# Kernel tuning notes

Measured on AMD Instinct MI355X. Metric: run time of the kernel, lower is better.

## Reference

```python
import jax, jax.numpy as jnp
import numpy as np

N_NODES = 50000
N_EDGES = 800000
IN_F = 128
HID = 64
HEADS = 4
N_CLASSES = 256
NEG_SLOPE = 0.2


def _gat_layer(h, W, al, ar, b, src, dst, act):
    """One DGL-style GATConv. h:[N,Din], W:[Din,H*F], al/ar:[H,F], b:[H*F].
    Returns [N,H,F]."""
    N = h.shape[0]
    H, F = al.shape
    z = (h @ W).reshape(N, H, F)                       # projected feats
    el = jnp.einsum('nhf,hf->nh', z, al)               # [N,H] src score part
    er = jnp.einsum('nhf,hf->nh', z, ar)               # [N,H] dst score part
    e = jax.nn.leaky_relu(el[src] + er[dst], negative_slope=NEG_SLOPE)  # [E,H]
    # segment softmax over incoming edges of each destination node
    emax = jax.ops.segment_max(e, dst, num_segments=N)                  # [N,H]
    ex = jnp.exp(e - emax[dst])                                         # [E,H]
    den = jax.ops.segment_sum(ex, dst, num_segments=N)                  # [N,H]
    alpha = ex / jnp.maximum(den[dst], 1e-9)                            # [E,H]
    msg = z[src] * alpha[:, :, None]                                    # [E,H,F]
    out = jax.ops.segment_sum(msg, dst, num_segments=N)                 # [N,H,F]
    out = out + b.reshape(1, H, F)
    return act(out) if act is not None else out


def setup_inputs() -> dict:
    key = jax.random.key(0)
    ks = jax.random.split(key, 16)
    feat = jax.random.normal(ks[0], (N_NODES, IN_F), dtype=jnp.float32)
    src = jax.random.randint(ks[1], (N_EDGES,), 0, N_NODES, dtype=jnp.int32)
    dst = jax.random.randint(ks[2], (N_EDGES,), 0, N_NODES, dtype=jnp.int32)

    def glorot(k, shape):
        fan = shape[0] + shape[-1]
        return jax.random.normal(k, shape, dtype=jnp.float32) * np.sqrt(2.0 / fan)

    # layer 0: IN_F -> HEADS*HID
    W0 = glorot(ks[3], (IN_F, HEADS * HID))
    al0 = glorot(ks[4], (HEADS, HID))
    ar0 = glorot(ks[5], (HEADS, HID))
    b0 = jnp.zeros((HEADS * HID,), dtype=jnp.float32)
    # layer 1: HEADS*HID -> HEADS*HID
    W1 = glorot(ks[6], (HEADS * HID, HEADS * HID))
    al1 = glorot(ks[7], (HEADS, HID))
    ar1 = glorot(ks[8], (HEADS, HID))
    b1 = jnp.zeros((HEADS * HID,), dtype=jnp.float32)
    # final layer: HEADS*HID -> HEADS*N_CLASSES
    W2 = glorot(ks[9], (HEADS * HID, HEADS * N_CLASSES))
    al2 = glorot(ks[10], (HEADS, N_CLASSES))
    ar2 = glorot(ks[11], (HEADS, N_CLASSES))
    b2 = jnp.zeros((HEADS * N_CLASSES,), dtype=jnp.float32)
    return {"feat": feat,
            "W0": W0, "al0": al0, "ar0": ar0, "b0": b0,
            "W1": W1, "al1": al1, "ar1": ar1, "b1": b1,
            "W2": W2, "al2": al2, "ar2": ar2, "b2": b2,
            "src": src, "dst": dst}


def reference(feat, W0, al0, ar0, b0, W1, al1, ar1, b1, W2, al2, ar2, b2, src, dst):
    elu = jax.nn.elu
    h = _gat_layer(feat, W0, al0, ar0, b0, src, dst, elu).reshape(N_NODES, -1)
    h = _gat_layer(h, W1, al1, ar1, b1, src, dst, elu).reshape(N_NODES, -1)
    logits = _gat_layer(h, W2, al2, ar2, b2, src, dst, None).mean(axis=1)  # [N, C]
    return logits
```

## Files before the change

kernel.cpp:

```cpp
#include <hip/hip_runtime.h>
#include <hip/hip_bf16.h>


#define NN 50000
#define NE 800000
#define NH_HEADS 4

typedef __attribute__((ext_vector_type(8))) short short8;
typedef __attribute__((ext_vector_type(8))) _Float16 half8;
typedef __attribute__((ext_vector_type(4))) _Float16 half4;
typedef __attribute__((ext_vector_type(4))) float floatx4;

__device__ inline float bf2f(short s) {
    union { unsigned u; float f; } v; v.u = ((unsigned)(unsigned short)s) << 16;
    return v.f;
}
__device__ inline short f2bf_rne(float x) {
    union { float f; unsigned u; } v; v.f = x;
    unsigned r = v.u + 0x7fff + ((v.u >> 16) & 1);
    return (short)(r >> 16);
}
__device__ inline void split1(float x, short& h, short& l) {
    union { float f; unsigned u; } v; v.f = x;
    h = (short)(v.u >> 16);
    union { float f; unsigned u; } rv; rv.f = v.f - bf2f(h);
    l = (short)(rv.u >> 16);
}

__device__ inline void load_lds16(const void* g, void* l) {
    __builtin_amdgcn_global_load_lds(
        (const __attribute__((address_space(1))) void*)g,
        (__attribute__((address_space(3))) void*)l, 16, 0, 0);
}


__global__ void hist_kernel(const int* __restrict__ dst, int* __restrict__ deg, int E) {
    int e = blockIdx.x * 256 + threadIdx.x;
    if (e < E) atomicAdd(&deg[dst[e]], 1);
}

__global__ void scan_block_kernel(const int* __restrict__ deg, int* __restrict__ offs,
                                  int* __restrict__ bsums, int n) {
    __shared__ int s[256];
    int tid = threadIdx.x;
    int i = blockIdx.x * 256 + tid;
    int v = (i < n) ? deg[i] : 0;
    s[tid] = v;
    __syncthreads();
    for (int off = 1; off < 256; off <<= 1) {
        int x = (tid >= off) ? s[tid - off] : 0;
        __syncthreads();
        s[tid] += x;
        __syncthreads();
    }
    if (i < n) offs[i] = s[tid] - v;
    if (tid == 255) bsums[blockIdx.x] = s[255];
}

__global__ void scan_sums_kernel(const int* __restrict__ bsums, int* __restrict__ boffs, int nb) {
    __shared__ int s[256];
    int tid = threadIdx.x;
    int v = (tid < nb) ? bsums[tid] : 0;
    s[tid] = v;
    __syncthreads();
    for (int off = 1; off < 256; off <<= 1) {
        int x = (tid >= off) ? s[tid - off] : 0;
        __syncthreads();
        s[tid] += x;
        __syncthreads();
    }
    boffs[tid] = s[tid] - v;
}

__global__ void add_offs_kernel(int* __restrict__ offs, const int* __restrict__ boffs,
                                int* __restrict__ cursor, int n, int total) {
    int i = blockIdx.x * 256 + threadIdx.x;
    if (i < n) {
        int o = offs[i] + boffs[blockIdx.x];
        offs[i] = o;
        cursor[i] = o;
    }
    if (i == 0) offs[n] = total;
}

__global__ void scatter_kernel(const int* __restrict__ src, const int* __restrict__ dst,
                               int* __restrict__ cursor, int* __restrict__ psrc, int E) {
    int e = blockIdx.x * 256 + threadIdx.x;
    if (e < E) {
        int p = atomicAdd(&cursor[dst[e]], 1);
        psrc[p] = src[e];
    }
}


__global__ __launch_bounds__(256) void splitA_rm(const float* __restrict__ A,
                                                 short* __restrict__ hi,
                                                 short* __restrict__ lo,
                                                 int total8) {
    int tid = blockIdx.x * 256 + threadIdx.x;
    if (tid >= total8) return;
    const float* p = A + (size_t)tid * 8;
    float4 x0 = ((const float4*)p)[0];
    float4 x1 = ((const float4*)p)[1];
    float xs[8] = {x0.x, x0.y, x0.z, x0.w, x1.x, x1.y, x1.z, x1.w};
    short8 hv, lv;
#pragma unroll
    for (int j = 0; j < 8; ++j) { short h, l; split1(xs[j], h, l); hv[j] = h; lv[j] = l; }
    ((short8*)hi)[tid] = hv;
    ((short8*)lo)[tid] = lv;
}


__global__ __launch_bounds__(256) void splitB_kernel(const float* __restrict__ B,
                                                     short* __restrict__ hi,
                                                     short* __restrict__ lo,
                                                     int K, int N) {
    int tid = blockIdx.x * 256 + threadIdx.x;
    int NG = N >> 4;
    int total = (K >> 5) * NG * 64;
    if (tid >= total) return;
    int lane = tid & 63;
    int rc = tid >> 6;
    int g = rc % NG, c = rc / NG;
    int n = g * 16 + (lane & 15);
    int k = c * 32 + (lane >> 4) * 8;
    short8 hv, lv;
#pragma unroll
    for (int j = 0; j < 8; ++j) {
        float x = B[(size_t)(k + j) * N + n];
        short h = f2bf_rne(x);
        hv[j] = h;
        lv[j] = f2bf_rne(x - bf2f(h));
    }
    ((short8*)hi)[tid] = hv;
    ((short8*)lo)[tid] = lv;
}

__global__ __launch_bounds__(256) void splitB_f16_kernel(const float* __restrict__ B,
                                                         _Float16* __restrict__ hi,
                                                         _Float16* __restrict__ lo,
                                                         int K, int N) {
    int tid = blockIdx.x * 256 + threadIdx.x;
    int NG = N >> 4;
    int total = (K >> 5) * NG * 64;
    if (tid >= total) return;
    int lane = tid & 63;
    int rc = tid >> 6;
    int g = rc % NG, c = rc / NG;
    int n = g * 16 + (lane & 15);
    int k = c * 32 + (lane >> 4) * 8;
    half8 hv, lv;
#pragma unroll
    for (int j = 0; j < 8; ++j) {
        float x = B[(size_t)(k + j) * N + n];
        _Float16 h = (_Float16)x;
        hv[j] = h;
        lv[j] = (_Float16)(x - (float)h);
    }
    ((half8*)hi)[tid] = hv;
    ((half8*)lo)[tid] = lv;
}

__global__ __launch_bounds__(256) void splitB2_f16s_kernel(const float* __restrict__ W2,
                                                           _Float16* __restrict__ hi) {
    int tid = blockIdx.x * 256 + threadIdx.x;
    const int NG = 16;
    int total = (1024 >> 5) * NG * 64;
    if (tid >= total) return;
    int lane = tid & 63;
    int rc = tid >> 6;
    int g = rc % NG, c = rc / NG;
    int n = g * 16 + (lane & 15);
    int kk = c * 32 + (lane >> 4) * 8;
    half8 hv;
#pragma unroll
    for (int j = 0; j < 8; ++j) {
        int kg = kk + j;
        int h = kg >> 8, k = kg & 255;
        hv[j] = (_Float16)W2[(size_t)k * 1024 + h * 256 + n];
    }
    ((half8*)hi)[tid] = hv;
}


__device__ inline floatx4 mfma16(short8 a, short8 b, floatx4 c) {
    return __builtin_amdgcn_mfma_f32_16x16x32_bf16(a, b, c, 0, 0, 0);
}
__device__ inline floatx4 mfma16h(half8 a, half8 b, floatx4 c) {
    return __builtin_amdgcn_mfma_f32_16x16x32_f16(a, b, c, 0, 0, 0);
}

__global__ __launch_bounds__(256) void gemm_n256l(const short* __restrict__ Ahi,
                                                  const short* __restrict__ Alo,
                                                  const short* __restrict__ Bh,
                                                  const short* __restrict__ Bl,
                                                  _Float16* __restrict__ Cf,
                                                  const float* __restrict__ alv,
                                                  const float* __restrict__ arv,
                                                  float* __restrict__ elo,
                                                  float* __restrict__ ero,
                                                  int M, int K) {
    int KC = K >> 5;
    __shared__ short AhL[2048];
    __shared__ short AlL[2048];
    int t = threadIdx.x;
    int lane = t & 63;
    int w = t >> 6;
    int bm = blockIdx.x * 64;
    int g0 = w * 4;
    const short8* pBh = (const short8*)Bh;
    const short8* pBl = (const short8*)Bl;

    floatx4 acc[4][4] = {};

    int row = bm + (w << 4) + (lane & 15);
    if (row >= M) row = M - 1;
    const short* gh = Ahi + (size_t)row * K + ((lane >> 4) << 3);
    const short* gl = Alo + (size_t)row * K + ((lane >> 4) << 3);
    short* lh = AhL + w * 512;
    short* ll = AlL + w * 512;

    for (int c = 0; c < KC; ++c) {
        load_lds16(gh + (size_t)c * 32, lh);
        load_lds16(gl + (size_t)c * 32, ll);
        short8 bh[4], bl[4];
#pragma unroll
        for (int g = 0; g < 4; ++g) {
            bh[g] = pBh[((size_t)c * 16 + g0 + g) * 64 + lane];
            bl[g] = pBl[((size_t)c * 16 + g0 + g) * 64 + lane];
        }
        __syncthreads();
#pragma unroll
        for (int mt = 0; mt < 4; ++mt) {
            short8 ah = *(const short8*)(AhL + mt * 512 + lane * 8);
            short8 al = *(const short8*)(AlL + mt * 512 + lane * 8);
#pragma unroll
            for (int g = 0; g < 4; ++g) {
                acc[mt][g] = mfma16(ah, bh[g], acc[mt][g]);
                acc[mt][g] = mfma16(al, bh[g], acc[mt][g]);
                acc[mt][g] = mfma16(ah, bl[g], acc[mt][g]);
            }
        }
        __syncthreads();
    }

    int rowb = bm + (lane >> 4) * 4;
    int colb = w * 64 + (lane & 15);
#pragma unroll
    for (int mt = 0; mt < 4; ++mt) {
#pragma unroll
        for (int r = 0; r < 4; ++r) {
            int rr = rowb + mt * 16 + r;
            if (rr < M) {
#pragma unroll
                for (int g = 0; g < 4; ++g) {
                    Cf[(size_t)rr * 256 + colb + g * 16] = (_Float16)acc[mt][g][r];
                }
            }
        }
    }

    if (alv) {
        float alr[4], arr_[4];
#pragma unroll
        for (int g = 0; g < 4; ++g) {
            int f = w * 64 + (lane & 15) + g * 16;
            alr[g] = alv[f];
            arr_[g] = arv[f];
        }
#pragma unroll
        for (int mt = 0; mt < 4; ++mt) {
#pragma unroll
            for (int r = 0; r < 4; ++r) {
                float se = acc[mt][0][r] * alr[0] + acc[mt][1][r] * alr[1] +
                           acc[mt][2][r] * alr[2] + acc[mt][3][r] * alr[3];
                float sr = acc[mt][0][r] * arr_[0] + acc[mt][1][r] * arr_[1] +
                           acc[mt][2][r] * arr_[2] + acc[mt][3][r] * arr_[3];
                se += __shfl_xor(se, 1); se += __shfl_xor(se, 2);
                se += __shfl_xor(se, 4); se += __shfl_xor(se, 8);
                sr += __shfl_xor(sr, 1); sr += __shfl_xor(sr, 2);
                sr += __shfl_xor(sr, 4); sr += __shfl_xor(sr, 8);
                int rr = rowb + mt * 16 + r;
                if ((lane & 15) == 0 && rr < M) {
                    elo[rr * 4 + w] = se;
                    ero[rr * 4 + w] = sr;
                }
            }
        }
    }
}

__global__ __launch_bounds__(256) void gemm_f16_n256(const _Float16* __restrict__ A,
                                                     const _Float16* __restrict__ Bh,
                                                     const _Float16* __restrict__ Bl,
                                                     const float* __restrict__ bias4,
                                                     float* __restrict__ C,
                                                     _Float16* __restrict__ Cf,
                                                     const float* __restrict__ alv,
                                                     const float* __restrict__ arv,
                                                     float* __restrict__ elo,
                                                     float* __restrict__ ero,
                                                     int M, int K) {
    int KC = K >> 5;
    __shared__ _Float16 AL[2048];
    int t = threadIdx.x;
    int lane = t & 63;
    int w = t >> 6;
    int bm = blockIdx.x * 64;
    int g0 = w * 4;
    const half8* pBh = (const half8*)Bh;
    const half8* pBl = (const half8*)Bl;
    bool dual = (Bl != nullptr);

    floatx4 acc[4][4] = {};

    int row = bm + (w << 4) + (lane & 15);
    if (row >= M) row = M - 1;
    const _Float16* gA = A + (size_t)row * K + ((lane >> 4) << 3);
    _Float16* lA = AL + w * 512;

    for (int c = 0; c < KC; ++c) {
        load_lds16(gA + (size_t)c * 32, lA);
        half8 bh[4], bl[4];
#pragma unroll
        for (int g = 0; g < 4; ++g) {
            bh[g] = pBh[((size_t)c * 16 + g0 + g) * 64 + lane];
        }
        if (dual) {
#pragma unroll
            for (int g = 0; g < 4; ++g) {
                bl[g] = pBl[((size_t)c * 16 + g0 + g) * 64 + lane];
            }
        }
        __syncthreads();
#pragma unroll
        for (int mt = 0; mt < 4; ++mt) {
            half8 a = *(const half8*)(AL + mt * 512 + lane * 8);
#pragma unroll
            for (int g = 0; g < 4; ++g) {
                acc[mt][g] = mfma16h(a, bh[g], acc[mt][g]);
            }
            if (dual) {
#pragma unroll
                for (int g = 0; g < 4; ++g) {
                    acc[mt][g] = mfma16h(a, bl[g], acc[mt][g]);
                }
            }
        }
        __syncthreads();
    }

    int rowb = bm + (lane >> 4) * 4;
    int colb = w * 64 + (lane & 15);
#pragma unroll
    for (int mt = 0; mt < 4; ++mt) {
#pragma unroll
        for (int r = 0; r < 4; ++r) {
            int rr = rowb + mt * 16 + r;
            if (rr < M) {
#pragma unroll
                for (int g = 0; g < 4; ++g) {
                    int col = colb + g * 16;
                    float v = acc[mt][g][r];
                    if (bias4) {
                        v = 0.25f * (v + bias4[col] + bias4[col + 256] +
                                     bias4[col + 512] + bias4[col + 768]);
                    }
                    if (Cf) Cf[(size_t)rr * 256 + col] = (_Float16)v;
                    else    C[(size_t)rr * 256 + col] = v;
                }
            }
        }
    }

    if (alv) {
        float alr[4], arr_[4];
#pragma unroll
        for (int g = 0; g < 4; ++g) {
            int f = w * 64 + (lane & 15) + g * 16;
            alr[g] = alv[f];
            arr_[g] = arv[f];
        }
#pragma unroll
        for (int mt = 0; mt < 4; ++mt) {
#pragma unroll
            for (int r = 0; r < 4; ++r) {
                float se = acc[mt][0][r] * alr[0] + acc[mt][1][r] * alr[1] +
                           acc[mt][2][r] * alr[2] + acc[mt][3][r] * alr[3];
                float sr = acc[mt][0][r] * arr_[0] + acc[mt][1][r] * arr_[1] +
                           acc[mt][2][r] * arr_[2] + acc[mt][3][r] * arr_[3];
                se += __shfl_xor(se, 1); se += __shfl_xor(se, 2);
                se += __shfl_xor(se, 4); se += __shfl_xor(se, 8);
                sr += __shfl_xor(sr, 1); sr += __shfl_xor(sr, 2);
                sr += __shfl_xor(sr, 4); sr += __shfl_xor(sr, 8);
                int rr = rowb + mt * 16 + r;
                if ((lane & 15) == 0 && rr < M) {
                    elo[rr * 4 + w] = se;
                    ero[rr * 4 + w] = sr;
                }
            }
        }
    }
}


__global__ __launch_bounds__(256) void proj_av_kernel(const float* __restrict__ W2,
                                                      const float* __restrict__ al2,
                                                      const float* __restrict__ ar2,
                                                      float* __restrict__ val,
                                                      float* __restrict__ var_) {
    int gid = blockIdx.x * 256 + threadIdx.x;
    int w = gid >> 6;
    int lane = threadIdx.x & 63;
    if (w >= 1024) return;
    int h = w >> 8, k = w & 255;
    const float* wrow = W2 + (size_t)k * 1024 + h * 256;
    const float* ap = al2 + h * 256;
    const float* rp = ar2 + h * 256;
    float sv = 0.f, sr = 0.f;
    for (int j = lane; j < 256; j += 64) {
        float x = wrow[j];
        sv += x * ap[j];
        sr += x * rp[j];
    }
#pragma unroll
    for (int off = 32; off > 0; off >>= 1) {
        sv += __shfl_down(sv, off);
        sr += __shfl_down(sr, off);
    }
    if (lane == 0) { val[w] = sv; var_[w] = sr; }
}

__global__ __launch_bounds__(256) void elr2_kernel(const _Float16* __restrict__ h1,
                                                   const float* __restrict__ val,
                                                   const float* __restrict__ var_,
                                                   float* __restrict__ el,
                                                   float* __restrict__ er) {
    int gid = blockIdx.x * 256 + threadIdx.x;
    int w = gid >> 6;
    int lane = threadIdx.x & 63;
    if (w >= NN * 4) return;
    int n = w >> 2, h = w & 3;
    const _Float16* hr = h1 + (size_t)n * 256;
    const float* vp = val + h * 256;
    const float* rp = var_ + h * 256;
    float se = 0.f, sr = 0.f;
    for (int k = lane; k < 256; k += 64) {
        float x = (float)hr[k];
        se += x * vp[k];
        sr += x * rp[k];
    }
#pragma unroll
    for (int off = 32; off > 0; off >>= 1) {
        se += __shfl_down(se, off);
        sr += __shfl_down(sr, off);
    }
    if (lane == 0) { el[w] = se; er[w] = sr; }
}


__global__ __launch_bounds__(64) void agg_z64_kernel(const _Float16* __restrict__ z,
                                                     const float* __restrict__ el,
                                                     const float* __restrict__ er,
                                                     const int* __restrict__ offs,
                                                     const int* __restrict__ psrc,
                                                     const float* __restrict__ bias,
                                                     _Float16* __restrict__ out) {
    int n = blockIdx.x;
    int l = threadIdx.x;
    __shared__ float p_lds[16][4];
    __shared__ int src_lds[16];
    __shared__ float den_lds[4];
    if (l < 4) den_lds[l] = 0.f;
    int e_local = l >> 2, hh = l & 3;
    int h = l >> 4;
    float er_n = er[n * 4 + hh];
    int beg = offs[n], end = offs[n + 1];
    float a0 = 0.f, a1 = 0.f, a2 = 0.f, a3 = 0.f;
    for (int base = beg; base < end; base += 16) {
        int cnt = min(16, end - base);
        __syncthreads();
        float p = 0.f;
        if (e_local < cnt) {
            int s = psrc[base + e_local];
            if (hh == 0) src_lds[e_local] = s;
            float sc = el[s * 4 + hh] + er_n;
            sc = (sc > 0.f) ? sc : 0.2f * sc;
            p = __expf(sc);
            p_lds[e_local][hh] = p;
        }
        float d = p;
        d += __shfl_xor(d, 4);  d += __shfl_xor(d, 8);
        d += __shfl_xor(d, 16); d += __shfl_xor(d, 32);
        if (l < 4) den_lds[l] += d;
        __syncthreads();
        for (int e = 0; e < cnt; ++e) {
            half4 v = *(const half4*)(z + (size_t)src_lds[e] * 256 + (l << 2));
            float pe = p_lds[e][h];
            a0 += pe * (float)v[0];
            a1 += pe * (float)v[1];
            a2 += pe * (float)v[2];
            a3 += pe * (float)v[3];
        }
    }
    __syncthreads();
    float rd = 1.f / fmaxf(den_lds[h], 1e-9f);
    float vals[4] = {a0, a1, a2, a3};
    half4 o;
#pragma unroll
    for (int j = 0; j < 4; ++j) {
        float x = vals[j] * rd + bias[(l << 2) + j];
        x = (x > 0.f) ? x : (__expf(x) - 1.f);
        o[j] = (_Float16)x;
    }
    *(half4*)(out + (size_t)n * 256 + (l << 2)) = o;
}

__global__ __launch_bounds__(64) void aggH_64_kernel(const _Float16* __restrict__ h1,
                                                     const float* __restrict__ el,
                                                     const float* __restrict__ er,
                                                     const int* __restrict__ offs,
                                                     const int* __restrict__ psrc,
                                                     _Float16* __restrict__ oA) {
    int n = blockIdx.x;
    int l = threadIdx.x;
    __shared__ __align__(16) float p_lds[16][4];
    __shared__ int src_lds[16];
    __shared__ float den_lds[4];
    if (l < 4) den_lds[l] = 0.f;
    int e_local = l >> 2, hh = l & 3;
    float er_n = er[n * 4 + hh];
    int beg = offs[n], end = offs[n + 1];
    float acc[4][4] = {};
    for (int base = beg; base < end; base += 16) {
        int cnt = min(16, end - base);
        __syncthreads();
        float p = 0.f;
        if (e_local < cnt) {
            int s = psrc[base + e_local];
            if (hh == 0) src_lds[e_local] = s;
            float sc = el[s * 4 + hh] + er_n;
            sc = (sc > 0.f) ? sc : 0.2f * sc;
            p = __expf(sc);
            p_lds[e_local][hh] = p;
        }
        float d = p;
        d += __shfl_xor(d, 4);  d += __shfl_xor(d, 8);
        d += __shfl_xor(d, 16); d += __shfl_xor(d, 32);
        if (l < 4) den_lds[l] += d;
        __syncthreads();
        for (int e = 0; e < cnt; ++e) {
            half4 v = *(const half4*)(h1 + (size_t)src_lds[e] * 256 + (l << 2));
            float vf0 = (float)v[0], vf1 = (float)v[1];
            float vf2 = (float)v[2], vf3 = (float)v[3];
            floatx4 pv = *(const floatx4*)&p_lds[e][0];
#pragma unroll
            for (int hd = 0; hd < 4; ++hd) {
                acc[hd][0] += pv[hd] * vf0;
                acc[hd][1] += pv[hd] * vf1;
                acc[hd][2] += pv[hd] * vf2;
                acc[hd][3] += pv[hd] * vf3;
            }
        }
    }
    __syncthreads();
    size_t base_o = (size_t)n * 1024 + (l << 2);
#pragma unroll
    for (int hd = 0; hd < 4; ++hd) {
        float rd = 1.f / fmaxf(den_lds[hd], 1e-9f);
        half4 o;
#pragma unroll
        for (int j = 0; j < 4; ++j) o[j] = (_Float16)(acc[hd][j] * rd);
        *(half4*)(oA + base_o + hd * 256) = o;
    }
}


extern "C" void kernel_launch(void* const* d_in, const int* in_sizes, int n_in,
                              void* d_out, int out_size, void* d_ws, size_t ws_size,
                              hipStream_t stream) {
    const float* feat = (const float*)d_in[0];
    const float* W0 = (const float*)d_in[1];
    const float* al0 = (const float*)d_in[2];
    const float* ar0 = (const float*)d_in[3];
    const float* b0 = (const float*)d_in[4];
    const float* W1 = (const float*)d_in[5];
    const float* al1 = (const float*)d_in[6];
    const float* ar1 = (const float*)d_in[7];
    const float* b1 = (const float*)d_in[8];
    const float* W2 = (const float*)d_in[9];
    const float* al2 = (const float*)d_in[10];
    const float* ar2 = (const float*)d_in[11];
    const float* b2 = (const float*)d_in[12];
    const int* src = (const int*)d_in[13];
    const int* dst = (const int*)d_in[14];
    float* out = (float*)d_out;

    float* slotA = (float*)d_ws;
    _Float16* zh = (_Float16*)slotA;
    short* feathi = (short*)(slotA + (size_t)NN * 256);
    short* featlo = feathi + (size_t)NN * 128;
    _Float16* Af16 = (_Float16*)slotA;
    float* slotB = slotA + (size_t)NN * 1024;
    _Float16* h0f = (_Float16*)slotB;
    _Float16* h1h = (_Float16*)slotB;
    float* el = slotB + (size_t)NN * 256;
    float* er = el + (size_t)NN * NH_HEADS;
    int* deg = (int*)(er + (size_t)NN * NH_HEADS);
    int* offs = deg + NN;
    int* cursor = offs + NN + 2;
    int* bsums = cursor + NN;
    int* boffs = bsums + 256;
    int* psrc = boffs + 256;
    short* Bh = (short*)(psrc + NE + 2);
    short* Bl = Bh + 262144;
    float* val = (float*)(Bl + 262144);
    float* var_ = val + 1024;

    hipMemsetAsync(deg, 0, NN * sizeof(int), stream);
    hist_kernel<<<(NE + 255) / 256, 256, 0, stream>>>(dst, deg, NE);
    int nb = (NN + 255) / 256;
    scan_block_kernel<<<nb, 256, 0, stream>>>(deg, offs, bsums, NN);
    scan_sums_kernel<<<1, 256, 0, stream>>>(bsums, boffs, nb);
    add_offs_kernel<<<nb, 256, 0, stream>>>(offs, boffs, cursor, NN, NE);
    scatter_kernel<<<(NE + 255) / 256, 256, 0, stream>>>(src, dst, cursor, psrc, NE);

    int mb64 = (NN + 63) / 64;

    splitA_rm<<<(NN * 128 / 8 + 255) / 256, 256, 0, stream>>>(feat, feathi, featlo, NN * 128 / 8);
    splitB_kernel<<<(4096 + 255) / 256, 256, 0, stream>>>(W0, Bh, Bl, 128, 256);
    gemm_n256l<<<mb64, 256, 0, stream>>>(feathi, featlo, Bh, Bl, zh,
                                         al0, ar0, el, er, NN, 128);
    agg_z64_kernel<<<NN, 64, 0, stream>>>(zh, el, er, offs, psrc, b0, h0f);

    splitB_f16_kernel<<<(8192 + 255) / 256, 256, 0, stream>>>(W1, (_Float16*)Bh,
                                                              (_Float16*)Bl, 256, 256);
    gemm_f16_n256<<<mb64, 256, 0, stream>>>(h0f, (const _Float16*)Bh, (const _Float16*)Bl,
                                            nullptr, nullptr, zh, al1, ar1, el, er,
                                            NN, 256);
    agg_z64_kernel<<<NN, 64, 0, stream>>>(zh, el, er, offs, psrc, b1, h1h);

    proj_av_kernel<<<256, 256, 0, stream>>>(W2, al2, ar2, val, var_);
    elr2_kernel<<<NN, 256, 0, stream>>>(h1h, val, var_, el, er);
    aggH_64_kernel<<<NN, 64, 0, stream>>>(h1h, el, er, offs, psrc, Af16);
    splitB2_f16s_kernel<<<(32768 + 255) / 256, 256, 0, stream>>>(W2, (_Float16*)Bh);
    gemm_f16_n256<<<mb64, 256, 0, stream>>>(Af16, (const _Float16*)Bh, nullptr,
                                            b2, out, nullptr, nullptr, nullptr,
                                            nullptr, nullptr, NN, 1024);
}
```

Baseline: 592.7 us.

## Store GEMM A operands in MFMA fragment layout and drop LDS staging

The producers of GEMM A operands (the feature split, the layer-0 aggregation output and the final-layer aggregation output) now write directly in a tiled MFMA-fragment order. The three GEMM kernels can then load A fragments straight into registers with coalesced 16-byte loads, with no LDS staging and no block barriers. This is meant to remove LDS traffic and syncthreads stalls in the GEMM main loops. In exchange, the aggregation kernels' output stores become scattered, and each wave now reloads all four A tiles instead of sharing one LDS copy, so global and L2 load traffic for A goes up.

Measured after the change: 668.6 us. 12.8% more time.

```diff
diff --git a/kernel.cpp b/kernel.cpp
--- a/kernel.cpp
+++ b/kernel.cpp
@@ -25,12 +25,6 @@
     h = (short)(v.u >> 16);
     union { float f; unsigned u; } rv; rv.f = v.f - bf2f(h);
     l = (short)(rv.u >> 16);
-}
-
-__device__ inline void load_lds16(const void* g, void* l) {
-    __builtin_amdgcn_global_load_lds(
-        (const __attribute__((address_space(1))) void*)g,
-        (__attribute__((address_space(3))) void*)l, 16, 0, 0);
 }
 
 
@@ -93,21 +87,23 @@
 }
 
 
-__global__ __launch_bounds__(256) void splitA_rm(const float* __restrict__ A,
-                                                 short* __restrict__ hi,
-                                                 short* __restrict__ lo,
-                                                 int total8) {
+__global__ __launch_bounds__(256) void splitA_perm(const float* __restrict__ A,
+                                                   short* __restrict__ hi,
+                                                   short* __restrict__ lo,
+                                                   int total) {
     int tid = blockIdx.x * 256 + threadIdx.x;
-    if (tid >= total8) return;
-    const float* p = A + (size_t)tid * 8;
+    if (tid >= total) return;
+    int n = tid >> 4, o = tid & 15;
+    const float* p = A + (size_t)n * 128 + o * 8;
     float4 x0 = ((const float4*)p)[0];
     float4 x1 = ((const float4*)p)[1];
     float xs[8] = {x0.x, x0.y, x0.z, x0.w, x1.x, x1.y, x1.z, x1.w};
     short8 hv, lv;
 #pragma unroll
     for (int j = 0; j < 8; ++j) { short h, l; split1(xs[j], h, l); hv[j] = h; lv[j] = l; }
-    ((short8*)hi)[tid] = hv;
-    ((short8*)lo)[tid] = lv;
+    size_t idx = ((size_t)(n >> 4) * 4 + (o >> 2)) * 64 + (n & 15) + 16 * (o & 3);
+    ((short8*)hi)[idx] = hv;
+    ((short8*)lo)[idx] = lv;
 }
 
 
@@ -201,47 +197,42 @@
                                                   float* __restrict__ ero,
                                                   int M, int K) {
     int KC = K >> 5;
-    __shared__ short AhL[2048];
-    __shared__ short AlL[2048];
     int t = threadIdx.x;
     int lane = t & 63;
     int w = t >> 6;
     int bm = blockIdx.x * 64;
+    int tile0 = blockIdx.x * 4;
     int g0 = w * 4;
+    const short8* pAh = (const short8*)Ahi;
+    const short8* pAl = (const short8*)Alo;
     const short8* pBh = (const short8*)Bh;
     const short8* pBl = (const short8*)Bl;
 
     floatx4 acc[4][4] = {};
 
-    int row = bm + (w << 4) + (lane & 15);
-    if (row >= M) row = M - 1;
-    const short* gh = Ahi + (size_t)row * K + ((lane >> 4) << 3);
-    const short* gl = Alo + (size_t)row * K + ((lane >> 4) << 3);
-    short* lh = AhL + w * 512;
-    short* ll = AlL + w * 512;
-
     for (int c = 0; c < KC; ++c) {
-        load_lds16(gh + (size_t)c * 32, lh);
-        load_lds16(gl + (size_t)c * 32, ll);
-        short8 bh[4], bl[4];
+        short8 ah[4], al4[4], bh[4], bl[4];
+#pragma unroll
+        for (int mt = 0; mt < 4; ++mt) {
+            size_t ia = ((size_t)(tile0 + mt) * KC + c) * 64 + lane;
+            ah[mt] = pAh[ia];
+            al4[mt] = pAl[ia];
+        }
 #pragma unroll
         for (int g = 0; g < 4; ++g) {
-            bh[g] = pBh[((size_t)c * 16 + g0 + g) * 64 + lane];
-            bl[g] = pBl[((size_t)c * 16 + g0 + g) * 64 + lane];
-        }
-        __syncthreads();
+            size_t ib = ((size_t)c * 16 + g0 + g) * 64 + lane;
+            bh[g] = pBh[ib];
+            bl[g] = pBl[ib];
+        }
 #pragma unroll
         for (int mt = 0; mt < 4; ++mt) {
-            short8 ah = *(const short8*)(AhL + mt * 512 + lane * 8);
-            short8 al = *(const short8*)(AlL + mt * 512 + lane * 8);
 #pragma unroll
             for (int g = 0; g < 4; ++g) {
-                acc[mt][g] = mfma16(ah, bh[g], acc[mt][g]);
-                acc[mt][g] = mfma16(al, bh[g], acc[mt][g]);
-                acc[mt][g] = mfma16(ah, bl[g], acc[mt][g]);
-            }
-        }
-        __syncthreads();
+                acc[mt][g] = mfma16(ah[mt], bh[g], acc[mt][g]);
+                acc[mt][g] = mfma16(al4[mt], bh[g], acc[mt][g]);
+                acc[mt][g] = mfma16(ah[mt], bl[g], acc[mt][g]);
+            }
+        }
     }
 
     int rowb = bm + (lane >> 4) * 4;
@@ -302,26 +293,25 @@
                                                      float* __restrict__ ero,
                                                      int M, int K) {
     int KC = K >> 5;
-    __shared__ _Float16 AL[2048];
     int t = threadIdx.x;
     int lane = t & 63;
     int w = t >> 6;
     int bm = blockIdx.x * 64;
+    int tile0 = blockIdx.x * 4;
     int g0 = w * 4;
+    const half8* pA = (const half8*)A;
     const half8* pBh = (const half8*)Bh;
     const half8* pBl = (const half8*)Bl;
     bool dual = (Bl != nullptr);
 
     floatx4 acc[4][4] = {};
 
-    int row = bm + (w << 4) + (lane & 15);
-    if (row >= M) row = M - 1;
-    const _Float16* gA = A + (size_t)row * K + ((lane >> 4) << 3);
-    _Float16* lA = AL + w * 512;
-
     for (int c = 0; c < KC; ++c) {
-        load_lds16(gA + (size_t)c * 32, lA);
-        half8 bh[4], bl[4];
+        half8 a[4], bh[4], bl[4];
+#pragma unroll
+        for (int mt = 0; mt < 4; ++mt) {
+            a[mt] = pA[((size_t)(tile0 + mt) * KC + c) * 64 + lane];
+        }
 #pragma unroll
         for (int g = 0; g < 4; ++g) {
             bh[g] = pBh[((size_t)c * 16 + g0 + g) * 64 + lane];
@@ -332,22 +322,19 @@
                 bl[g] = pBl[((size_t)c * 16 + g0 + g) * 64 + lane];
             }
         }
-        __syncthreads();
 #pragma unroll
         for (int mt = 0; mt < 4; ++mt) {
-            half8 a = *(const half8*)(AL + mt * 512 + lane * 8);
 #pragma unroll
             for (int g = 0; g < 4; ++g) {
-                acc[mt][g] = mfma16h(a, bh[g], acc[mt][g]);
+                acc[mt][g] = mfma16h(a[mt], bh[g], acc[mt][g]);
             }
             if (dual) {
 #pragma unroll
                 for (int g = 0; g < 4; ++g) {
-                    acc[mt][g] = mfma16h(a, bl[g], acc[mt][g]);
+                    acc[mt][g] = mfma16h(a[mt], bl[g], acc[mt][g]);
                 }
             }
         }
-        __syncthreads();
     }
 
     int rowb = bm + (lane >> 4) * 4;
@@ -465,7 +452,8 @@
                                                      const int* __restrict__ offs,
                                                      const int* __restrict__ psrc,
                                                      const float* __restrict__ bias,
-                                                     _Float16* __restrict__ out) {
+                                                     _Float16* __restrict__ out,
+                                                     int perm) {
     int n = blockIdx.x;
     int l = threadIdx.x;
     __shared__ float p_lds[16][4];
@@ -513,7 +501,13 @@
         x = (x > 0.f) ? x : (__expf(x) - 1.f);
         o[j] = (_Float16)x;
     }
-    *(half4*)(out + (size_t)n * 256 + (l << 2)) = o;
+    if (perm) {
+        size_t off = ((((size_t)(n >> 4) * 8 + (l >> 3)) * 64 +
+                       (n & 15) + 16 * ((l >> 1) & 3)) << 3) + ((l & 1) << 2);
+        *(half4*)(out + off) = o;
+    } else {
+        *(half4*)(out + (size_t)n * 256 + (l << 2)) = o;
+    }
 }
 
 __global__ __launch_bounds__(64) void aggH_64_kernel(const _Float16* __restrict__ h1,
@@ -564,14 +558,17 @@
         }
     }
     __syncthreads();
-    size_t base_o = (size_t)n * 1024 + (l << 2);
+    size_t tb = (size_t)(n >> 4) * 32;
+    int lane_in = (n & 15) + 16 * ((l >> 1) & 3);
+    int j0 = (l & 1) << 2;
 #pragma unroll
     for (int hd = 0; hd < 4; ++hd) {
         float rd = 1.f / fmaxf(den_lds[hd], 1e-9f);
         half4 o;
 #pragma unroll
         for (int j = 0; j < 4; ++j) o[j] = (_Float16)(acc[hd][j] * rd);
-        *(half4*)(oA + base_o + hd * 256) = o;
+        size_t off = (((tb + hd * 8 + (l >> 3)) * 64 + lane_in) << 3) + j0;
+        *(half4*)(oA + off) = o;
     }
 }
 
@@ -596,10 +593,13 @@
     const int* dst = (const int*)d_in[14];
     float* out = (float*)d_out;
 
+    int mb64 = (NN + 63) / 64;
+    size_t TIL = (size_t)mb64 * 4;
+
     float* slotA = (float*)d_ws;
     _Float16* zh = (_Float16*)slotA;
     short* feathi = (short*)(slotA + (size_t)NN * 256);
-    short* featlo = feathi + (size_t)NN * 128;
+    short* featlo = feathi + TIL * 4 * 512;
     _Float16* Af16 = (_Float16*)slotA;
     float* slotB = slotA + (size_t)NN * 1024;
     _Float16* h0f = (_Float16*)slotB;
@@ -625,20 +625,18 @@
     add_offs_kernel<<<nb, 256, 0, stream>>>(offs, boffs, cursor, NN, NE);
     scatter_kernel<<<(NE + 255) / 256, 256, 0, stream>>>(src, dst, cursor, psrc, NE);
 
-    int mb64 = (NN + 63) / 64;
-
-    splitA_rm<<<(NN * 128 / 8 + 255) / 256, 256, 0, stream>>>(feat, feathi, featlo, NN * 128 / 8);
+    splitA_perm<<<(NN * 16 + 255) / 256, 256, 0, stream>>>(feat, feathi, featlo, NN * 16);
     splitB_kernel<<<(4096 + 255) / 256, 256, 0, stream>>>(W0, Bh, Bl, 128, 256);
     gemm_n256l<<<mb64, 256, 0, stream>>>(feathi, featlo, Bh, Bl, zh,
                                          al0, ar0, el, er, NN, 128);
-    agg_z64_kernel<<<NN, 64, 0, stream>>>(zh, el, er, offs, psrc, b0, h0f);
+    agg_z64_kernel<<<NN, 64, 0, stream>>>(zh, el, er, offs, psrc, b0, h0f, 1);
 
     splitB_f16_kernel<<<(8192 + 255) / 256, 256, 0, stream>>>(W1, (_Float16*)Bh,
                                                               (_Float16*)Bl, 256, 256);
     gemm_f16_n256<<<mb64, 256, 0, stream>>>(h0f, (const _Float16*)Bh, (const _Float16*)Bl,
                                             nullptr, nullptr, zh, al1, ar1, el, er,
                                             NN, 256);
-    agg_z64_kernel<<<NN, 64, 0, stream>>>(zh, el, er, offs, psrc, b1, h1h);
+    agg_z64_kernel<<<NN, 64, 0, stream>>>(zh, el, er, offs, psrc, b1, h1h, 0);
 
     proj_av_kernel<<<256, 256, 0, stream>>>(W2, al2, ar2, val, var_);
     elr2_kernel<<<NN, 256, 0, stream>>>(h1h, val, var_, el, er);
```
